# Kernel optimization log

Hardware: AMD Instinct MI355X
Metric: run time of the kernel (lower is better)

## Reference

```python
import jax, jax.numpy as jnp
import numpy as np

EMBED_DIM = 1024
N_HEADS = 16
HEAD_SIZE = EMBED_DIM // N_HEADS
SCALE = HEAD_SIZE ** -0.5


def setup_inputs() -> dict:
    key = jax.random.key(0)
    ks = jax.random.split(key, 11)
    B, Tq, Tk, C = 4, 1024, 1024, EMBED_DIM
    std = 0.02
    return {
        "q": jax.random.normal(ks[0], (B, Tq, C), jnp.float32),
        "k": jax.random.normal(ks[1], (B, Tk, C), jnp.float32),
        "v": jax.random.normal(ks[2], (B, Tk, C), jnp.float32),
        "Wq": jax.random.normal(ks[3], (C, C), jnp.float32) * std,
        "bq": jnp.zeros((C,), jnp.float32),
        "Wk": jax.random.normal(ks[4], (C, C), jnp.float32) * std,
        "bk": jnp.zeros((C,), jnp.float32),
        "Wv": jax.random.normal(ks[5], (C, C), jnp.float32) * std,
        "bv": jnp.zeros((C,), jnp.float32),
        "Wo": jax.random.normal(ks[6], (C, C), jnp.float32) * std,
        "bo": jnp.zeros((C,), jnp.float32),
    }


def reference(q, k, v, Wq, bq, Wk, bk, Wv, bv, Wo, bo):
    b, t, c = q.shape
    # linear projections (torch Linear: x @ W.T + b)
    qp = q @ Wq.T + bq            # [b, tq, c]
    kp = k @ Wk.T + bk            # [b, tk, c]
    vp = v @ Wv.T + bv            # [b, tk, c]
    # split heads: [b, h, t, d]
    qh = qp.reshape(b, t, N_HEADS, HEAD_SIZE).transpose(0, 2, 1, 3)
    kh = kp.reshape(b, kp.shape[1], N_HEADS, HEAD_SIZE).transpose(0, 2, 1, 3)
    vh = vp.reshape(b, vp.shape[1], N_HEADS, HEAD_SIZE).transpose(0, 2, 1, 3)
    # scaled dot-product attention
    scores = jnp.einsum('bhqd,bhkd->bhqk', qh, kh) * SCALE
    weights = jax.nn.softmax(scores, axis=-1)
    attn = jnp.einsum('bhqk,bhkd->bhqd', weights, vh)
    attn = attn.transpose(0, 2, 1, 3).reshape(b, t, c)
    out = attn @ Wo.T + bo
    return out
```

## Files before the change

### kernel.cpp

```cpp
#include <hip/hip_runtime.h>
#include <stdint.h>

typedef unsigned short u16;
typedef unsigned int   u32;
typedef __bf16 bf16;
typedef bf16  bf16x2 __attribute__((ext_vector_type(2)));
typedef bf16  bf16x8 __attribute__((ext_vector_type(8)));
typedef float f32x4  __attribute__((ext_vector_type(4)));

#define AS1 __attribute__((address_space(1)))
#define AS3 __attribute__((address_space(3)))


__device__ __forceinline__ u32 pk2(float lo, float hi) {
  bf16x2 t;
  t[0] = (bf16)lo;
  t[1] = (bf16)hi;
  return __builtin_bit_cast(u32, t);
}

__device__ __forceinline__ u16 b1(float f) {
  bf16 t = (bf16)f;
  return __builtin_bit_cast(u16, t);
}

__device__ __forceinline__ void gload_lds16(const void* src, void* dst) {
  __builtin_amdgcn_global_load_lds((const AS1 void*)src, (AS3 void*)dst, 16, 0, 0);
}

__device__ __forceinline__ bf16x8 fragL(const char* lds, int row, int kbyte) {
  return *(const bf16x8*)(lds + row * 128 + kbyte);
}


__global__ __launch_bounds__(256) void cvt_w(
    const float* wq, const float* wk, const float* wv, const float* wo,
    u16* wqb, u16* wkb, u16* wvb, u16* wob)
{
  const float* src; u16* dst;
  switch (blockIdx.y) {
    case 0: src = wq; dst = wqb; break;
    case 1: src = wk; dst = wkb; break;
    case 2: src = wv; dst = wvb; break;
    default: src = wo; dst = wob; break;
  }
  const int n4 = 262144;
  int stride = gridDim.x * blockDim.x;
  for (int i = blockIdx.x * blockDim.x + threadIdx.x; i < n4; i += stride) {
    float4 f = ((const float4*)src)[i];
    uint2 o;
    o.x = pk2(f.x, f.y);
    o.y = pk2(f.z, f.w);
    ((uint2*)dst)[i] = o;
  }
}


__device__ __forceinline__ void stageL(const u16* gtile, char* lds, int tid)
{
  int w = tid >> 6, lane = tid & 63;
  int rr = lane >> 3;
  int cb = (lane & 7) << 4;
  #pragma unroll
  for (int i = 0; i < 4; ++i) {
    int c = i * 4 + w;
    gload_lds16((const char*)(gtile + (c * 8 + rr) * 1024) + cb, lds + c * 1024);
  }
}

__device__ __forceinline__ void stageA_f32(const float* gA, char* lds, int tid)
{
  int r0 = tid >> 3;
  int c8 = (tid & 7) << 3;
  #pragma unroll
  for (int i = 0; i < 4; ++i) {
    int r = i * 32 + r0;
    const float* p = gA + r * 1024 + c8;
    float4 f0 = *(const float4*)p;
    float4 f1 = *(const float4*)(p + 4);
    uint4 o;
    o.x = pk2(f0.x, f0.y);
    o.y = pk2(f0.z, f0.w);
    o.z = pk2(f1.x, f1.y);
    o.w = pk2(f1.z, f1.w);
    *(uint4*)(lds + r * 128 + (c8 << 1)) = o;
  }
}

__device__ __forceinline__ void mfma_tile(const char* As, const char* Bs,
                                          f32x4 acc[4][4], int lane,
                                          int wr, int wc)
{
  #pragma unroll
  for (int ks = 0; ks < 2; ++ks) {
    int kb = ks * 64 + ((lane >> 4) << 4);
    bf16x8 af[4], bfr[4];
    #pragma unroll
    for (int m = 0; m < 4; ++m) af[m]  = fragL(As, wr * 64 + m * 16 + (lane & 15), kb);
    #pragma unroll
    for (int n = 0; n < 4; ++n) bfr[n] = fragL(Bs, wc * 64 + n * 16 + (lane & 15), kb);
    #pragma unroll
    for (int m = 0; m < 4; ++m)
      #pragma unroll
      for (int n = 0; n < 4; ++n)
        acc[m][n] = __builtin_amdgcn_mfma_f32_16x16x32_bf16(af[m], bfr[n], acc[m][n], 0, 0, 0);
  }
}


__global__ __launch_bounds__(256, 2) void proj_gemm(
    const float* qf, const float* kf, const float* vf,
    const u16* wqb, const u16* wkb, const u16* wvb,
    const float* bq, const float* bk, const float* bv,
    u16* qh, u16* kh, u16* vt)
{
  __shared__ alignas(16) char As[16384];
  __shared__ alignas(16) char Bs[16384];
  int tid = threadIdx.x;
  int bi = blockIdx.x & 31, bj = blockIdx.x >> 5;
  int z = blockIdx.z;
  const float* A = (z == 0) ? qf : (z == 1) ? kf : vf;
  const u16* W = (z == 0) ? wqb : (z == 1) ? wkb : wvb;
  const float* bias = (z == 0) ? bq : (z == 1) ? bk : bv;
  u16* dst = (z == 0) ? qh : (z == 1) ? kh : vt;

  int lane = tid & 63;
  int wr = (tid >> 7) & 1, wc = (tid >> 6) & 1;
  f32x4 acc[4][4] = {};
  for (int kt = 0; kt < 16; ++kt) {
    stageA_f32(A + bi * 131072 + kt * 64, As, tid);
    stageL(W + bj * 131072 + kt * 64, Bs, tid);
    __syncthreads();
    mfma_tile(As, Bs, acc, lane, wr, wc);
    __syncthreads();
  }

  int rbase = bi * 128 + wr * 64 + ((lane >> 4) << 2);
  int cbase = bj * 128 + wc * 64;
  #pragma unroll
  for (int n = 0; n < 4; ++n) {
    int col = cbase + n * 16 + (lane & 15);
    float bsv = bias[col];
    int h = col >> 6, d = col & 63;
    #pragma unroll
    for (int m = 0; m < 4; ++m) {
      #pragma unroll
      for (int r = 0; r < 4; ++r) {
        int R = rbase + m * 16 + r;
        int b = R >> 10, t = R & 1023;
        u16 val = b1(acc[m][n][r] + bsv);
        if (z < 2) dst[(((b * 16 + h) * 1024 + t) << 6) + d] = val;
        else       dst[(((b * 16 + h) * 64 + d) << 10) + t] = val;
      }
    }
  }
}


__global__ __launch_bounds__(256, 2) void out_gemm(
    const u16* attn, const u16* wob, const float* bo, float* out)
{
  __shared__ alignas(16) char As[16384];
  __shared__ alignas(16) char Bs[16384];
  int tid = threadIdx.x;
  int bi = blockIdx.x & 31, bj = blockIdx.x >> 5;

  int lane = tid & 63;
  int wr = (tid >> 7) & 1, wc = (tid >> 6) & 1;
  f32x4 acc[4][4] = {};
  for (int kt = 0; kt < 16; ++kt) {
    stageL(attn + bi * 131072 + kt * 64, As, tid);
    stageL(wob  + bj * 131072 + kt * 64, Bs, tid);
    __syncthreads();
    mfma_tile(As, Bs, acc, lane, wr, wc);
    __syncthreads();
  }

  int rbase = bi * 128 + wr * 64 + ((lane >> 4) << 2);
  int cbase = bj * 128 + wc * 64;
  #pragma unroll
  for (int n = 0; n < 4; ++n) {
    int col = cbase + n * 16 + (lane & 15);
    float bsv = bo[col];
    #pragma unroll
    for (int m = 0; m < 4; ++m) {
      #pragma unroll
      for (int r = 0; r < 4; ++r) {
        int R = rbase + m * 16 + r;
        out[R * 1024 + col] = acc[m][n][r] + bsv;
      }
    }
  }
}


__global__ __launch_bounds__(256, 2) void attn_fwd(
    const u16* qh, const u16* kh, const u16* vt, u16* attnb)
{
  __shared__ alignas(16) u16 Ks[64 * 72];
  __shared__ alignas(16) u16 Vs[64 * 72];
  __shared__ alignas(16) u16 Pl[4][16 * 72];

  const float SC = 0.125f;
  const float RTHR = 64.0f;

  int tid = threadIdx.x, lane = tid & 63, w = tid >> 6;
  int g = lane >> 4;
  int q0 = blockIdx.x << 6;
  int bh = blockIdx.y;
  const u16* qbase = qh + bh * 65536;
  const u16* kbase = kh + bh * 65536;
  const u16* vbase = vt + bh * 65536;

  bf16x8 qf[2];
  {
    int qrow = q0 + w * 16 + (lane & 15);
    const u16* p = qbase + qrow * 64 + (g << 3);
    qf[0] = *(const bf16x8*)p;
    qf[1] = *(const bf16x8*)(p + 32);
  }

  f32x4 ot[4] = {};
  float m_r = -3.0e38f, l_r = 0.f;

  int sr = tid >> 2;
  int sj = (tid & 3) << 4;
  u16* pw = Pl[w];
  int prow = (lane & 15) * 72;

  for (int kv0 = 0; kv0 < 1024; kv0 += 64) {
    {
      const u16* ksrc = kbase + (kv0 + sr) * 64 + sj;
      const u16* vsrc = vbase + sr * 1024 + kv0 + sj;
      *(bf16x8*)(Ks + sr * 72 + sj)     = *(const bf16x8*)ksrc;
      *(bf16x8*)(Ks + sr * 72 + sj + 8) = *(const bf16x8*)(ksrc + 8);
      *(bf16x8*)(Vs + sr * 72 + sj)     = *(const bf16x8*)vsrc;
      *(bf16x8*)(Vs + sr * 72 + sj + 8) = *(const bf16x8*)(vsrc + 8);
    }
    __syncthreads();

    f32x4 sc[4] = {};
    #pragma unroll
    for (int ks = 0; ks < 2; ++ks) {
      #pragma unroll
      for (int m = 0; m < 4; ++m) {
        bf16x8 kf = *(const bf16x8*)(Ks + (m * 16 + (lane & 15)) * 72 + ks * 32 + g * 8);
        sc[m] = __builtin_amdgcn_mfma_f32_16x16x32_bf16(kf, qf[ks], sc[m], 0, 0, 0);
      }
    }

    float vmax = -3.0e38f;
    #pragma unroll
    for (int m = 0; m < 4; ++m)
      #pragma unroll
      for (int r = 0; r < 4; ++r)
        vmax = fmaxf(vmax, sc[m][r]);
    vmax = fmaxf(vmax, __shfl_xor(vmax, 16, 64));
    vmax = fmaxf(vmax, __shfl_xor(vmax, 32, 64));

    if (!__all(vmax - m_r <= RTHR)) {
      float mnew = fmaxf(m_r, vmax);
      float fac = __expf((m_r - mnew) * SC);
      l_r *= fac;
      #pragma unroll
      for (int dm = 0; dm < 4; ++dm) ot[dm] *= fac;
      m_r = mnew;
    }
    float nm = -m_r * SC;

    float psum = 0.f;
    u32 pp[4][2];
    #pragma unroll
    for (int m = 0; m < 4; ++m) {
      float p0 = __expf(fmaf(sc[m][0], SC, nm));
      float p1 = __expf(fmaf(sc[m][1], SC, nm));
      float p2 = __expf(fmaf(sc[m][2], SC, nm));
      float p3 = __expf(fmaf(sc[m][3], SC, nm));
      psum += (p0 + p1) + (p2 + p3);
      pp[m][0] = pk2(p0, p1);
      pp[m][1] = pk2(p2, p3);
    }
    psum += __shfl_xor(psum, 16, 64);
    psum += __shfl_xor(psum, 32, 64);
    l_r += psum;

    #pragma unroll
    for (int m = 0; m < 4; ++m) {
      u32* d = (u32*)(pw + prow + m * 16 + (g << 2));
      d[0] = pp[m][0];
      d[1] = pp[m][1];
    }

    #pragma unroll
    for (int ks = 0; ks < 2; ++ks) {
      bf16x8 pf = *(const bf16x8*)(pw + prow + ks * 32 + g * 8);
      #pragma unroll
      for (int dm = 0; dm < 4; ++dm) {
        bf16x8 vf = *(const bf16x8*)(Vs + (dm * 16 + (lane & 15)) * 72 + ks * 32 + g * 8);
        ot[dm] = __builtin_amdgcn_mfma_f32_16x16x32_bf16(vf, pf, ot[dm], 0, 0, 0);
      }
    }
    __syncthreads();
  }

  float inv = 1.0f / l_r;
  int b = bh >> 4, h = bh & 15;
  int tok = (b << 10) + q0 + w * 16 + (lane & 15);
  u16* obase = attnb + tok * 1024 + h * 64;
  #pragma unroll
  for (int dm = 0; dm < 4; ++dm) {
    int d0 = dm * 16 + (g << 2);
    u32* d = (u32*)(obase + d0);
    d[0] = pk2(ot[dm][0] * inv, ot[dm][1] * inv);
    d[1] = pk2(ot[dm][2] * inv, ot[dm][3] * inv);
  }
}


extern "C" void kernel_launch(void* const* d_in, const int* in_sizes, int n_in,
                              void* d_out, int out_size, void* d_ws, size_t ws_size,
                              hipStream_t stream)
{
  const float* q  = (const float*)d_in[0];
  const float* k  = (const float*)d_in[1];
  const float* v  = (const float*)d_in[2];
  const float* Wq = (const float*)d_in[3];
  const float* bq = (const float*)d_in[4];
  const float* Wk = (const float*)d_in[5];
  const float* bk = (const float*)d_in[6];
  const float* Wv = (const float*)d_in[7];
  const float* bv = (const float*)d_in[8];
  const float* Wo = (const float*)d_in[9];
  const float* bo = (const float*)d_in[10];
  float* out = (float*)d_out;

  u16* ws  = (u16*)d_ws;
  u16* wqb = ws;
  u16* wkb = wqb + (1u << 20);
  u16* wvb = wkb + (1u << 20);
  u16* wob = wvb + (1u << 20);
  u16* qhb = wob + (1u << 20);
  u16* khb = qhb + (4u << 20);
  u16* vtb = khb + (4u << 20);
  u16* atb = vtb + (4u << 20);

  cvt_w<<<dim3(256, 4, 1), 256, 0, stream>>>(Wq, Wk, Wv, Wo, wqb, wkb, wvb, wob);
  proj_gemm<<<dim3(256, 1, 3), 256, 0, stream>>>(q, k, v, wqb, wkb, wvb,
                                                 bq, bk, bv, qhb, khb, vtb);
  attn_fwd<<<dim3(16, 64, 1), 256, 0, stream>>>(qhb, khb, vtb, atb);
  out_gemm<<<dim3(256, 1, 1), 256, 0, stream>>>(atb, wob, bo, out);
}
```

Baseline: 238.5 us.

## Shrink GEMM tiles to 64x128, swizzle LDS, and prefetch fp32 A into registers

The projection and output GEMMs move from 128x128 to 64x128 tiles, which doubles the grid to 512 blocks per GEMM and raises the occupancy target to 4 blocks per CU. The LDS layout gains an XOR swizzle on 16-byte chunks, applied to global_load_lds staging, register writes and fragment reads, to cut bank conflicts. In proj_gemm the fp32 A tile for the next k-step is loaded into registers while the current step computes, hiding global latency. Smaller tiles lower per-block data reuse and raise total global traffic for the weight operand.

```diff
diff --git a/kernel.cpp b/kernel.cpp
--- a/kernel.cpp
+++ b/kernel.cpp
@@ -28,8 +28,8 @@
   __builtin_amdgcn_global_load_lds((const AS1 void*)src, (AS3 void*)dst, 16, 0, 0);
 }
 
-__device__ __forceinline__ bf16x8 fragL(const char* lds, int row, int kbyte) {
-  return *(const bf16x8*)(lds + row * 128 + kbyte);
+__device__ __forceinline__ bf16x8 fragS(const char* lds, int row, int kbyte) {
+  return *(const bf16x8*)(lds + row * 128 + (kbyte ^ ((row & 7) << 4)));
 }
 
 
@@ -56,51 +56,63 @@
 }
 
 
-__device__ __forceinline__ void stageL(const u16* gtile, char* lds, int tid)
+template<int NC>
+__device__ __forceinline__ void stageSw(const u16* gtile, char* lds, int tid)
 {
   int w = tid >> 6, lane = tid & 63;
   int rr = lane >> 3;
   int cb = (lane & 7) << 4;
   #pragma unroll
-  for (int i = 0; i < 4; ++i) {
+  for (int i = 0; i < NC; ++i) {
     int c = i * 4 + w;
-    gload_lds16((const char*)(gtile + (c * 8 + rr) * 1024) + cb, lds + c * 1024);
-  }
-}
-
-__device__ __forceinline__ void stageA_f32(const float* gA, char* lds, int tid)
-{
-  int r0 = tid >> 3;
-  int c8 = (tid & 7) << 3;
-  #pragma unroll
-  for (int i = 0; i < 4; ++i) {
+    int r = c * 8 + rr;
+    gload_lds16((const char*)(gtile + r * 1024) + (cb ^ (rr << 4)), lds + c * 1024);
+  }
+}
+
+__device__ __forceinline__ void loadA64(const float* gA, int tid,
+                                        float4* pa, float4* pb)
+{
+  int r0 = tid >> 3, c8 = (tid & 7) << 3;
+  #pragma unroll
+  for (int i = 0; i < 2; ++i) {
+    const float* p = gA + (i * 32 + r0) * 1024 + c8;
+    pa[i] = *(const float4*)p;
+    pb[i] = *(const float4*)(p + 4);
+  }
+}
+
+__device__ __forceinline__ void writeA64(char* lds, int tid,
+                                         const float4* pa, const float4* pb)
+{
+  int r0 = tid >> 3, cb = (tid & 7) << 4;
+  #pragma unroll
+  for (int i = 0; i < 2; ++i) {
     int r = i * 32 + r0;
-    const float* p = gA + r * 1024 + c8;
-    float4 f0 = *(const float4*)p;
-    float4 f1 = *(const float4*)(p + 4);
     uint4 o;
-    o.x = pk2(f0.x, f0.y);
-    o.y = pk2(f0.z, f0.w);
-    o.z = pk2(f1.x, f1.y);
-    o.w = pk2(f1.z, f1.w);
-    *(uint4*)(lds + r * 128 + (c8 << 1)) = o;
-  }
-}
-
-__device__ __forceinline__ void mfma_tile(const char* As, const char* Bs,
-                                          f32x4 acc[4][4], int lane,
-                                          int wr, int wc)
-{
+    o.x = pk2(pa[i].x, pa[i].y);
+    o.y = pk2(pa[i].z, pa[i].w);
+    o.z = pk2(pb[i].x, pb[i].y);
+    o.w = pk2(pb[i].z, pb[i].w);
+    *(uint4*)(lds + r * 128 + (cb ^ ((r & 7) << 4))) = o;
+  }
+}
+
+__device__ __forceinline__ void mfma_64x128(const char* As, const char* Bs,
+                                            f32x4 acc[2][4], int lane,
+                                            int wr, int wc)
+{
+  int g = lane >> 4;
   #pragma unroll
   for (int ks = 0; ks < 2; ++ks) {
-    int kb = ks * 64 + ((lane >> 4) << 4);
-    bf16x8 af[4], bfr[4];
-    #pragma unroll
-    for (int m = 0; m < 4; ++m) af[m]  = fragL(As, wr * 64 + m * 16 + (lane & 15), kb);
-    #pragma unroll
-    for (int n = 0; n < 4; ++n) bfr[n] = fragL(Bs, wc * 64 + n * 16 + (lane & 15), kb);
-    #pragma unroll
-    for (int m = 0; m < 4; ++m)
+    int kb = ks * 64 + (g << 4);
+    bf16x8 af[2], bfr[4];
+    #pragma unroll
+    for (int m = 0; m < 2; ++m) af[m]  = fragS(As, wr * 32 + m * 16 + (lane & 15), kb);
+    #pragma unroll
+    for (int n = 0; n < 4; ++n) bfr[n] = fragS(Bs, wc * 64 + n * 16 + (lane & 15), kb);
+    #pragma unroll
+    for (int m = 0; m < 2; ++m)
       #pragma unroll
       for (int n = 0; n < 4; ++n)
         acc[m][n] = __builtin_amdgcn_mfma_f32_16x16x32_bf16(af[m], bfr[n], acc[m][n], 0, 0, 0);
@@ -108,16 +120,16 @@
 }
 
 
-__global__ __launch_bounds__(256, 2) void proj_gemm(
+__global__ __launch_bounds__(256, 4) void proj_gemm(
     const float* qf, const float* kf, const float* vf,
     const u16* wqb, const u16* wkb, const u16* wvb,
     const float* bq, const float* bk, const float* bv,
     u16* qh, u16* kh, u16* vt)
 {
-  __shared__ alignas(16) char As[16384];
+  __shared__ alignas(16) char As[8192];
   __shared__ alignas(16) char Bs[16384];
   int tid = threadIdx.x;
-  int bi = blockIdx.x & 31, bj = blockIdx.x >> 5;
+  int bi = blockIdx.x & 63, bj = blockIdx.x >> 6;
   int z = blockIdx.z;
   const float* A = (z == 0) ? qf : (z == 1) ? kf : vf;
   const u16* W = (z == 0) ? wqb : (z == 1) ? wkb : wvb;
@@ -126,16 +138,22 @@
 
   int lane = tid & 63;
   int wr = (tid >> 7) & 1, wc = (tid >> 6) & 1;
-  f32x4 acc[4][4] = {};
+
+  float4 pa[2], pb[2];
+  loadA64(A + bi * 65536, tid, pa, pb);
+
+  f32x4 acc[2][4] = {};
   for (int kt = 0; kt < 16; ++kt) {
-    stageA_f32(A + bi * 131072 + kt * 64, As, tid);
-    stageL(W + bj * 131072 + kt * 64, Bs, tid);
-    __syncthreads();
-    mfma_tile(As, Bs, acc, lane, wr, wc);
-    __syncthreads();
-  }
-
-  int rbase = bi * 128 + wr * 64 + ((lane >> 4) << 2);
+    writeA64(As, tid, pa, pb);
+    stageSw<4>(W + bj * 131072 + kt * 64, Bs, tid);
+    if (kt < 15)
+      loadA64(A + bi * 65536 + (kt + 1) * 64, tid, pa, pb);
+    __syncthreads();
+    mfma_64x128(As, Bs, acc, lane, wr, wc);
+    __syncthreads();
+  }
+
+  int rbase = bi * 64 + wr * 32 + ((lane >> 4) << 2);
   int cbase = bj * 128 + wc * 64;
   #pragma unroll
   for (int n = 0; n < 4; ++n) {
@@ -143,7 +161,7 @@
     float bsv = bias[col];
     int h = col >> 6, d = col & 63;
     #pragma unroll
-    for (int m = 0; m < 4; ++m) {
+    for (int m = 0; m < 2; ++m) {
       #pragma unroll
       for (int r = 0; r < 4; ++r) {
         int R = rbase + m * 16 + r;
@@ -157,33 +175,33 @@
 }
 
 
-__global__ __launch_bounds__(256, 2) void out_gemm(
+__global__ __launch_bounds__(256, 4) void out_gemm(
     const u16* attn, const u16* wob, const float* bo, float* out)
 {
-  __shared__ alignas(16) char As[16384];
+  __shared__ alignas(16) char As[8192];
   __shared__ alignas(16) char Bs[16384];
   int tid = threadIdx.x;
-  int bi = blockIdx.x & 31, bj = blockIdx.x >> 5;
+  int bi = blockIdx.x & 63, bj = blockIdx.x >> 6;
 
   int lane = tid & 63;
   int wr = (tid >> 7) & 1, wc = (tid >> 6) & 1;
-  f32x4 acc[4][4] = {};
+  f32x4 acc[2][4] = {};
   for (int kt = 0; kt < 16; ++kt) {
-    stageL(attn + bi * 131072 + kt * 64, As, tid);
-    stageL(wob  + bj * 131072 + kt * 64, Bs, tid);
-    __syncthreads();
-    mfma_tile(As, Bs, acc, lane, wr, wc);
-    __syncthreads();
-  }
-
-  int rbase = bi * 128 + wr * 64 + ((lane >> 4) << 2);
+    stageSw<2>(attn + bi * 65536  + kt * 64, As, tid);
+    stageSw<4>(wob  + bj * 131072 + kt * 64, Bs, tid);
+    __syncthreads();
+    mfma_64x128(As, Bs, acc, lane, wr, wc);
+    __syncthreads();
+  }
+
+  int rbase = bi * 64 + wr * 32 + ((lane >> 4) << 2);
   int cbase = bj * 128 + wc * 64;
   #pragma unroll
   for (int n = 0; n < 4; ++n) {
     int col = cbase + n * 16 + (lane & 15);
     float bsv = bo[col];
     #pragma unroll
-    for (int m = 0; m < 4; ++m) {
+    for (int m = 0; m < 2; ++m) {
       #pragma unroll
       for (int r = 0; r < 4; ++r) {
         int R = rbase + m * 16 + r;
@@ -345,8 +363,8 @@
   u16* atb = vtb + (4u << 20);
 
   cvt_w<<<dim3(256, 4, 1), 256, 0, stream>>>(Wq, Wk, Wv, Wo, wqb, wkb, wvb, wob);
-  proj_gemm<<<dim3(256, 1, 3), 256, 0, stream>>>(q, k, v, wqb, wkb, wvb,
+  proj_gemm<<<dim3(512, 1, 3), 256, 0, stream>>>(q, k, v, wqb, wkb, wvb,
                                                  bq, bk, bv, qhb, khb, vtb);
   attn_fwd<<<dim3(16, 64, 1), 256, 0, stream>>>(qhb, khb, vtb, atb);
-  out_gemm<<<dim3(256, 1, 1), 256, 0, stream>>>(atb, wob, bo, out);
-}
+  out_gemm<<<dim3(512, 1, 1), 256, 0, stream>>>(atb, wob, bo, out);
+}
```

After: 223.5 us. -6.3%, faster.
